# Optimization experiments

Hardware: AMD Instinct MI355X
Metric: run time of the kernel (lower is better)

The kernel has to match this reference:

```python
import jax, jax.numpy as jnp
import numpy as np

EPS = 1e-5
MAX_NORM = 1.0 - 1e-4

def _artanh(x):
    x = jnp.clip(x, -1.0 + 1e-5, 1.0 - 1e-5)
    return 0.5 * (jnp.log1p(x) - jnp.log1p(-x))

def _norm(x):
    return jnp.sqrt(jnp.maximum(jnp.sum(x * x, axis=-1, keepdims=True), EPS * EPS))

def _project(x):
    # clip points into the Poincare ball (c=1)
    n = _norm(x)
    return x * jnp.minimum(1.0, MAX_NORM / n)

def _logmap0(x):
    n = _norm(x)
    return _artanh(n) * x / n

def _expmap0(v):
    n = _norm(v)
    return jnp.tanh(n) * v / n

def _mobius_add(x, y):
    x2 = jnp.sum(x * x, -1, keepdims=True)
    y2 = jnp.sum(y * y, -1, keepdims=True)
    xy = jnp.sum(x * y, -1, keepdims=True)
    num = (1.0 + 2.0 * xy + y2) * x + (1.0 - x2) * y
    den = 1.0 + 2.0 * xy + x2 * y2
    return num / jnp.maximum(den, EPS)

def _mobius_matvec_all(W, x):
    # x: [B,T,D] on ball, W: [K,D,D] -> [B,T,K,D] (mx = x @ W[k].T for each expert k)
    mx = jnp.einsum('btd,ked->btke', x, W)
    xn = _norm(x)[:, :, None, :]            # [B,T,1,1]
    mn = _norm(mx)                          # [B,T,K,1]
    return jnp.tanh(mn / xn * _artanh(xn)) * mx / mn

def _depthwise_conv1d(x, w, b):
    # x: [B,T,C], w: [C,1,3] depthwise, padding=1
    y = jax.lax.conv_general_dilated(
        jnp.transpose(x, (0, 2, 1)), w, (1,), 'SAME',
        feature_group_count=x.shape[-1],
        dimension_numbers=('NCW', 'OIW', 'NCW'))
    return jnp.transpose(y, (0, 2, 1)) + b

def setup_inputs() -> dict:
    key = jax.random.key(0)
    ks = jax.random.split(key, 10)
    B, T, V, D, K, E, R = 8, 512, 50257, 64, 17, 32, 40
    return {
        'tokens': jax.random.randint(ks[0], (B, T), 0, V),
        'token_embed': 0.02 * jax.random.normal(ks[1], (V, D), jnp.float32),
        'conv_w': 0.3 * jax.random.normal(ks[2], (D, 1, 3), jnp.float32),
        'conv_b': jnp.zeros((D,), jnp.float32),
        'lin_w': 0.1 * jax.random.normal(ks[3], (D, K), jnp.float32),
        'lin_b': jnp.zeros((K,), jnp.float32),
        'exp_W': (1.0 / 8.0) * jax.random.normal(ks[4], (K, D, D), jnp.float32),
        'exp_bias': 0.01 * jax.random.normal(ks[5], (K, D), jnp.float32),
        'ln_gamma': jnp.ones((K, E), jnp.float32),
        'ln_beta': jnp.zeros((K, E), jnp.float32),
        'rel_T': jax.random.normal(ks[6], (R, E, E), jnp.float32),
        'rel_S': jax.random.normal(ks[7], (R, E, E), jnp.float32),
    }

def reference(tokens, token_embed, conv_w, conv_b, lin_w, lin_b,
              exp_W, exp_bias, ln_gamma, ln_beta, rel_T, rel_S):
    B, T = tokens.shape
    h0 = token_embed[tokens]                                  # [B,T,64]
    # TinyPosRouter: depthwise conv -> linear -> log_softmax
    hc = _depthwise_conv1d(h0, conv_w, conv_b)
    logp = jax.nn.log_softmax(hc @ lin_w + lin_b, axis=-1)    # [B,T,17]
    p = jnp.exp(logp)
    # round-trip through tangent space (as in source)
    x = _expmap0(_logmap0(_project(h0)))                      # [B,T,64]
    # all 17 hyperbolic experts, batched
    mv = _mobius_matvec_all(exp_W, x)                         # [B,T,17,64]
    y = _project(_mobius_add(mv, _project(exp_bias)))         # mobius bias add
    yt = _logmap0(y)                                          # tangent [B,T,17,64]
    a, g = jnp.split(yt, 2, axis=-1)
    y_glu = a * jax.nn.sigmoid(g)                             # [B,T,17,32]
    mu = jnp.mean(y_glu, -1, keepdims=True)
    var = jnp.var(y_glu, -1, keepdims=True)
    y_ln = (y_glu - mu) / jnp.sqrt(var + 1e-5) * ln_gamma + ln_beta
    y_out = _expmap0(y_ln)                                    # [B,T,17,32]
    y_avg = jnp.einsum('btke,btk->bte', y_out, p)             # soft routing
    # per-relation biaffine scores
    Th = jnp.einsum('btd,rde->brte', y_avg, rel_T)            # [B,40,T,32]
    Sd = jnp.einsum('btd,rde->brte', y_avg, rel_S)
    scores = jnp.einsum('brid,brjd->brij', Th, Sd) / Th.shape[-1]  # [B,40,T,T]
    score_rel = jnp.max(scores, axis=1)                       # [B,T,T]
    score_rel = jnp.where(jnp.eye(T, dtype=bool)[None], -1e9, score_rel)
    # greedy arborescence approximation: each dependent picks max-scoring head
    tree = jnp.argmax(score_rel, axis=1)                      # [B,T]
    return tree, score_rel, logp
```

## Files before the change

### kernel.cpp

```cpp
#include <hip/hip_runtime.h>
#include <hip/hip_bf16.h>
#include <math.h>

#define EPS   1e-5f
#define EPS2  (1e-5f * 1e-5f)
#define MAXN  (1.0f - 1e-4f)

typedef __attribute__((ext_vector_type(8))) short bf16x8;
typedef __attribute__((ext_vector_type(4))) float f32x4;

__device__ __forceinline__ float artanh_(float x) {
    x = fminf(fmaxf(x, -1.0f + 1e-5f), 1.0f - 1e-5f);
    return 0.5f * (log1pf(x) - log1pf(-x));
}
__device__ __forceinline__ float redw(float v) {
    #pragma unroll
    for (int m = 32; m >= 1; m >>= 1) v += __shfl_xor(v, m);
    return v;
}
__device__ __forceinline__ float red16(float v) {
    v += __shfl_xor(v, 1); v += __shfl_xor(v, 2);
    v += __shfl_xor(v, 4); v += __shfl_xor(v, 8);
    return v;
}
__device__ __forceinline__ float red8(float v) {
    v += __shfl_xor(v, 1); v += __shfl_xor(v, 2); v += __shfl_xor(v, 4);
    return v;
}
__device__ __forceinline__ float sigmoid_(float z) { return 1.0f / (1.0f + expf(-z)); }
__device__ __forceinline__ ushort f2bf(float f) {
    union { __hip_bfloat16 b; ushort u; } cv;
    cv.b = __float2bfloat16(f);
    return cv.u;
}
__device__ __forceinline__ bf16x8 pack8(float4 lo, float4 hi) {
    bf16x8 r;
    r[0] = (short)f2bf(lo.x); r[1] = (short)f2bf(lo.y);
    r[2] = (short)f2bf(lo.z); r[3] = (short)f2bf(lo.w);
    r[4] = (short)f2bf(hi.x); r[5] = (short)f2bf(hi.y);
    r[6] = (short)f2bf(hi.z); r[7] = (short)f2bf(hi.w);
    return r;
}

__global__ __launch_bounds__(256) void k1_token(
    const int* __restrict__ tokens, const float* __restrict__ emb,
    const float* __restrict__ conv_w, const float* __restrict__ conv_b,
    const float* __restrict__ lin_w, const float* __restrict__ lin_b,
    float* __restrict__ x_out, float* __restrict__ xn_out,
    float* __restrict__ p_out, float* __restrict__ logp_out)
{
    const int tok = blockIdx.x * 4 + (threadIdx.x >> 6);
    const int t   = tok & 511;
    const int c   = threadIdx.x & 63;

    const int id0 = tokens[tok];
    float h0 = emb[id0 * 64 + c];
    float hm = 0.0f, hp = 0.0f;
    if (t > 0)   hm = emb[tokens[tok - 1] * 64 + c];
    if (t < 511) hp = emb[tokens[tok + 1] * 64 + c];

    float hc = conv_w[c * 3 + 0] * hm + conv_w[c * 3 + 1] * h0 +
               conv_w[c * 3 + 2] * hp + conv_b[c];

    float myLg = 0.0f;
    #pragma unroll
    for (int j = 0; j < 17; ++j) {
        float v = redw(hc * lin_w[c * 17 + j]);
        if (c == j) myLg = v + lin_b[j];
    }
    float mx = (c < 17) ? myLg : -1e30f;
    #pragma unroll
    for (int m = 32; m >= 1; m >>= 1) mx = fmaxf(mx, __shfl_xor(mx, m));
    float ev = (c < 17) ? expf(myLg - mx) : 0.0f;
    float se = redw(ev);
    float lse = logf(se);
    if (c < 17) {
        float lp = myLg - mx - lse;
        logp_out[tok * 17 + c] = lp;
        p_out[tok * 17 + c]    = expf(lp);
    }

    float n0 = sqrtf(fmaxf(redw(h0 * h0), EPS2));
    float xp = h0 * fminf(1.0f, MAXN / n0);
    float n1 = sqrtf(fmaxf(redw(xp * xp), EPS2));
    float v1 = artanh_(n1) / n1 * xp;
    float n2 = sqrtf(fmaxf(redw(v1 * v1), EPS2));
    float xv = tanhf(n2) / n2 * v1;

    x_out[tok * 64 + c] = xv;
    float n3 = sqrtf(fmaxf(redw(xv * xv), EPS2));
    if (c == 0) xn_out[tok] = n3;
}

__global__ __launch_bounds__(256) void k2_expert(
    const float* __restrict__ x_in, const float* __restrict__ xn_in,
    const float* __restrict__ p_in, const float* __restrict__ expW,
    const float* __restrict__ expB, const float* __restrict__ g_in,
    const float* __restrict__ b_in, __hip_bfloat16* __restrict__ yk_out)
{
    __shared__ float mv_s[16][65];
    __shared__ float pb[64];
    __shared__ float gsk[32], bsk[32];
    __shared__ float p_sk[16];
    __shared__ float xn_s[16], axn_s[16];
    __shared__ float y2s_s;

    const int tid = threadIdx.x;
    const int l = tid & 63, w = tid >> 6;
    const int tg = tid >> 4, eg = tid & 15;
    const int k = blockIdx.x >> 8;
    const int chunk = blockIdx.x & 255;
    const int tok0 = chunk * 16;

    {
        const int d0 = (l >> 4) * 8;
        const float* ap = x_in + (tok0 + (l & 15)) * 64 + d0;
        const float* bp = expW + k * 4096 + (16 * w + (l & 15)) * 64 + d0;
        bf16x8 a0 = pack8(*reinterpret_cast<const float4*>(ap),
                          *reinterpret_cast<const float4*>(ap + 4));
        bf16x8 a1 = pack8(*reinterpret_cast<const float4*>(ap + 32),
                          *reinterpret_cast<const float4*>(ap + 36));
        bf16x8 b0 = pack8(*reinterpret_cast<const float4*>(bp),
                          *reinterpret_cast<const float4*>(bp + 4));
        bf16x8 b1 = pack8(*reinterpret_cast<const float4*>(bp + 32),
                          *reinterpret_cast<const float4*>(bp + 36));
        f32x4 acc = {0.f, 0.f, 0.f, 0.f};
        acc = __builtin_amdgcn_mfma_f32_16x16x32_bf16(a0, b0, acc, 0, 0, 0);
        acc = __builtin_amdgcn_mfma_f32_16x16x32_bf16(a1, b1, acc, 0, 0, 0);
        #pragma unroll
        for (int q = 0; q < 4; ++q)
            mv_s[(l >> 4) * 4 + q][16 * w + (l & 15)] = acc[q];
    }

    if (tid < 64) {
        float wv = expB[k * 64 + tid];
        float s = redw(wv * wv);
        float n = sqrtf(fmaxf(s, EPS2));
        float sc = fminf(1.0f, MAXN / n);
        pb[tid] = wv * sc;
        if (tid == 0) y2s_s = s * sc * sc;
    }
    if (tid >= 64 && tid < 96)  gsk[tid - 64] = g_in[k * 32 + (tid - 64)];
    if (tid >= 96 && tid < 128) bsk[tid - 96] = b_in[k * 32 + (tid - 96)];
    if (tid >= 128 && tid < 144) p_sk[tid - 128] = p_in[(tok0 + tid - 128) * 17 + k];
    if (tid >= 144 && tid < 160) {
        float xn = xn_in[tok0 + tid - 144];
        xn_s[tid - 144] = xn;
        axn_s[tid - 144] = artanh_(xn);
    }
    __syncthreads();

    const float xnv = xn_s[tg], axnv = axn_s[tg];
    float4 mvq = *reinterpret_cast<const float4*>(&mv_s[tg][eg * 4]);
    float mv0 = mvq.x, mv1 = mvq.y, mv2 = mvq.z, mv3 = mvq.w;

    float mn = sqrtf(fmaxf(red16(mv0*mv0 + mv1*mv1 + mv2*mv2 + mv3*mv3), EPS2));
    float tv = tanhf(mn / xnv * axnv);
    float cf = tv / mn;
    float xa0 = cf * mv0, xa1 = cf * mv1, xa2 = cf * mv2, xa3 = cf * mv3;
    float x2 = tv * tv;

    float4 pbv = *reinterpret_cast<const float4*>(&pb[eg * 4]);
    float xy = red16(xa0*pbv.x + xa1*pbv.y + xa2*pbv.z + xa3*pbv.w);
    float y2 = y2s_s;
    float ca = 1.0f + 2.0f * xy + y2;
    float cb = 1.0f - x2;
    float den = fmaxf(1.0f + 2.0f * xy + x2 * y2, EPS);
    float rden = 1.0f / den;
    float y0 = (ca * xa0 + cb * pbv.x) * rden;
    float y1 = (ca * xa1 + cb * pbv.y) * rden;
    float y2c = (ca * xa2 + cb * pbv.z) * rden;
    float y3 = (ca * xa3 + cb * pbv.w) * rden;

    float s2 = red16(y0*y0 + y1*y1 + y2c*y2c + y3*y3);
    float nP = sqrtf(fmaxf(s2, EPS2));
    float scP = fminf(1.0f, MAXN / nP);
    y0 *= scP; y1 *= scP; y2c *= scP; y3 *= scP;

    float n2 = sqrtf(fmaxf(s2 * scP * scP, EPS2));
    float lc = artanh_(n2) / n2;
    float yt0 = lc * y0, yt1 = lc * y1, yt2 = lc * y2c, yt3 = lc * y3;

    float pr0 = __shfl_xor(yt0, 8), pr1 = __shfl_xor(yt1, 8);
    float pr2 = __shfl_xor(yt2, 8), pr3 = __shfl_xor(yt3, 8);
    float gl0, gl1, gl2, gl3;
    if (eg < 8) {
        gl0 = yt0 * sigmoid_(pr0); gl1 = yt1 * sigmoid_(pr1);
        gl2 = yt2 * sigmoid_(pr2); gl3 = yt3 * sigmoid_(pr3);
    } else {
        gl0 = pr0 * sigmoid_(yt0); gl1 = pr1 * sigmoid_(yt1);
        gl2 = pr2 * sigmoid_(yt2); gl3 = pr3 * sigmoid_(yt3);
    }

    float mu = red8(gl0 + gl1 + gl2 + gl3) * (1.0f / 32.0f);
    float sq = red8(gl0*gl0 + gl1*gl1 + gl2*gl2 + gl3*gl3) * (1.0f / 32.0f);
    float rstd = rsqrtf(fmaxf(sq - mu * mu, 0.0f) + 1e-5f);
    int c0 = 4 * (eg & 7);
    float ln0 = (gl0 - mu) * rstd * gsk[c0 + 0] + bsk[c0 + 0];
    float ln1 = (gl1 - mu) * rstd * gsk[c0 + 1] + bsk[c0 + 1];
    float ln2 = (gl2 - mu) * rstd * gsk[c0 + 2] + bsk[c0 + 2];
    float ln3 = (gl3 - mu) * rstd * gsk[c0 + 3] + bsk[c0 + 3];

    float n3 = sqrtf(fmaxf(red8(ln0*ln0 + ln1*ln1 + ln2*ln2 + ln3*ln3), EPS2));
    float tc = tanhf(n3) / n3;

    float pk = p_sk[tg];
    float wq = pk * tc;

    if (eg < 8) {
        int tok = tok0 + tg;
        ushort4 o;
        o.x = f2bf(wq * ln0);
        o.y = f2bf(wq * ln1);
        o.z = f2bf(wq * ln2);
        o.w = f2bf(wq * ln3);
        *reinterpret_cast<ushort4*>(
            reinterpret_cast<ushort*>(yk_out) + ((size_t)tok * 17 + k) * 32 + c0) = o;
    }
}

__global__ __launch_bounds__(256) void k3_reduce(
    const __hip_bfloat16* __restrict__ yk, ushort* __restrict__ yab)
{
    int idx = blockIdx.x * 256 + threadIdx.x;
    int tok = idx >> 5, e = idx & 31;
    const __hip_bfloat16* p = yk + (size_t)tok * 17 * 32 + e;
    float s = 0.0f;
    #pragma unroll
    for (int k = 0; k < 17; ++k) s += __bfloat162float(p[k * 32]);
    yab[idx] = f2bf(s);
}

__global__ __launch_bounds__(256) void k4_rel(
    const ushort* __restrict__ yab, const float* __restrict__ relT,
    const float* __restrict__ relS, ushort* __restrict__ Z,
    unsigned long long* __restrict__ pmax)
{
    const int blk = blockIdx.x;
    const int b = blk / 160;
    const int rem = blk % 160;
    const int r = rem >> 2, tq = rem & 3;
    __shared__ float Ts[32][33], Ss[32][33], Mm[32][33];
    __shared__ float Zb[128][33];
    const int tid = threadIdx.x;
    const int l = tid & 63, w = tid >> 6;

    if (r == 0 && tid < 128)
        pmax[(size_t)b * 512 + tq * 128 + tid] = 0ull;

    {
        int d = tid >> 3, e0 = (tid & 7) * 4;
        float4 wT = *reinterpret_cast<const float4*>(&relT[r * 1024 + tid * 4]);
        float4 wS = *reinterpret_cast<const float4*>(&relS[r * 1024 + tid * 4]);
        Ts[d][e0 + 0] = wT.x; Ts[d][e0 + 1] = wT.y;
        Ts[d][e0 + 2] = wT.z; Ts[d][e0 + 3] = wT.w;
        Ss[d][e0 + 0] = wS.x; Ss[d][e0 + 1] = wS.y;
        Ss[d][e0 + 2] = wS.z; Ss[d][e0 + 3] = wS.w;
    }
    __syncthreads();

    {
        int d = tid >> 3, dp0 = (tid & 7) * 4;
        float m0 = 0.f, m1 = 0.f, m2 = 0.f, m3 = 0.f;
        #pragma unroll
        for (int e = 0; e < 32; ++e) {
            float tvv = Ts[d][e];
            m0 = fmaf(tvv, Ss[dp0 + 0][e], m0);
            m1 = fmaf(tvv, Ss[dp0 + 1][e], m1);
            m2 = fmaf(tvv, Ss[dp0 + 2][e], m2);
            m3 = fmaf(tvv, Ss[dp0 + 3][e], m3);
        }
        Mm[d][dp0 + 0] = m0; Mm[d][dp0 + 1] = m1;
        Mm[d][dp0 + 2] = m2; Mm[d][dp0 + 3] = m3;
    }
    __syncthreads();

    bf16x8 bm0, bm1;
    #pragma unroll
    for (int i = 0; i < 8; ++i) {
        int d = (l >> 4) * 8 + i;
        bm0[i] = (short)f2bf(Mm[d][(l & 15)]);
        bm1[i] = (short)f2bf(Mm[d][16 + (l & 15)]);
    }

    #pragma unroll
    for (int s = 0; s < 2; ++s) {
        int trow = tq * 128 + (w * 2 + s) * 16 + (l & 15);
        bf16x8 a = *reinterpret_cast<const bf16x8*>(
            yab + ((size_t)(b * 512) + trow) * 32 + (l >> 4) * 8);
        f32x4 acc0 = {0.f, 0.f, 0.f, 0.f}, acc1 = {0.f, 0.f, 0.f, 0.f};
        acc0 = __builtin_amdgcn_mfma_f32_16x16x32_bf16(a, bm0, acc0, 0, 0, 0);
        acc1 = __builtin_amdgcn_mfma_f32_16x16x32_bf16(a, bm1, acc1, 0, 0, 0);
        #pragma unroll
        for (int q = 0; q < 4; ++q) {
            int lr = (w * 2 + s) * 16 + (l >> 4) * 4 + q;
            Zb[lr][(l & 15)]      = acc0[q];
            Zb[lr][16 + (l & 15)] = acc1[q];
        }
    }
    __syncthreads();

    {
        int t2 = tid >> 1, half = tid & 1;
        union { ushort u[16]; uint4 q[2]; } pk;
        #pragma unroll
        for (int j = 0; j < 16; ++j) pk.u[j] = f2bf(Zb[t2][half * 16 + j]);
        size_t off = ((size_t)(b * 40 + r) * 512 + tq * 128 + t2) * 32 + half * 16;
        *reinterpret_cast<uint4*>(Z + off)     = pk.q[0];
        *reinterpret_cast<uint4*>(Z + off + 8) = pk.q[1];
    }
}

__global__ __launch_bounds__(1024) void k5_scores(
    const ushort* __restrict__ Z, const ushort* __restrict__ yab,
    float* __restrict__ score_out, unsigned long long* __restrict__ pmax)
{
    __shared__ float L[4][64][64];
    __shared__ unsigned long long pk_s[16][64];

    const int blk = blockIdx.x;
    const int b = blk >> 6, tile = blk & 63;
    const int it = (tile >> 3) * 64, jt = (tile & 7) * 64;
    const int w = threadIdx.x >> 6, lane = threadIdx.x & 63;
    const int q = w >> 2, s = w & 3;
    const int i0 = it + s * 16;
    const int arow = i0 + (lane & 15);
    const int koff = (lane >> 4) * 8;

    bf16x8 bb[4];
    #pragma unroll
    for (int c = 0; c < 4; ++c) {
        int jrow = jt + c * 16 + (lane & 15);
        bb[c] = *reinterpret_cast<const bf16x8*>(
            yab + ((size_t)(b * 512) + jrow) * 32 + koff);
    }

    f32x4 runmax[4];
    #pragma unroll
    for (int c = 0; c < 4; ++c)
        #pragma unroll
        for (int qq = 0; qq < 4; ++qq) runmax[c][qq] = -3.0e38f;

    const int r0 = q * 10;
    #pragma unroll 2
    for (int r = r0; r < r0 + 10; ++r) {
        bf16x8 a = *reinterpret_cast<const bf16x8*>(
            Z + ((size_t)(b * 40 + r) * 512 + arow) * 32 + koff);
        #pragma unroll
        for (int c = 0; c < 4; ++c) {
            f32x4 acc = {0.f, 0.f, 0.f, 0.f};
            acc = __builtin_amdgcn_mfma_f32_16x16x32_bf16(a, bb[c], acc, 0, 0, 0);
            #pragma unroll
            for (int qq = 0; qq < 4; ++qq) runmax[c][qq] = fmaxf(runmax[c][qq], acc[qq]);
        }
    }

    #pragma unroll
    for (int c = 0; c < 4; ++c) {
        #pragma unroll
        for (int qq = 0; qq < 4; ++qq) {
            int li = s * 16 + (lane >> 4) * 4 + qq;
            int lj = c * 16 + (lane & 15);
            L[q][li][lj] = runmax[c][qq];
        }
    }
    __syncthreads();

    {
        const int jl = threadIdx.x & 63, ig = threadIdx.x >> 6;
        const int gj = jt + jl;
        float bestv = -3.0e38f; int besti = it;
        #pragma unroll
        for (int p = 0; p < 4; ++p) {
            int i = ig + p * 16;
            float v = fmaxf(fmaxf(L[0][i][jl], L[1][i][jl]),
                            fmaxf(L[2][i][jl], L[3][i][jl])) * (1.0f / 32.0f);
            int gi = it + i;
            if (gi == gj) v = -1e9f;
            score_out[((size_t)b * 512 + gi) * 512 + gj] = v;
            if (v > bestv) { bestv = v; besti = gi; }
        }
        unsigned int ub = __float_as_uint(bestv);
        unsigned int ok = (ub >> 31) ? ~ub : (ub | 0x80000000u);
        pk_s[ig][jl] = ((unsigned long long)ok << 32) | (unsigned int)(511 - besti);
    }
    __syncthreads();
    if (threadIdx.x < 64) {
        unsigned long long best = pk_s[0][threadIdx.x];
        #pragma unroll
        for (int g = 1; g < 16; ++g) {
            unsigned long long v = pk_s[g][threadIdx.x];
            if (v > best) best = v;
        }
        atomicMax(&pmax[(size_t)b * 512 + jt + threadIdx.x], best);
    }
}

__global__ __launch_bounds__(256) void k6_tree(
    const unsigned long long* __restrict__ pmax, float* __restrict__ tree)
{
    int idx = blockIdx.x * 256 + threadIdx.x;
    tree[idx] = (float)(511 - (int)(pmax[idx] & 0x1ffull));
}

extern "C" void kernel_launch(void* const* d_in, const int* in_sizes, int n_in,
                              void* d_out, int out_size, void* d_ws, size_t ws_size,
                              hipStream_t stream)
{
    const int*   tokens  = (const int*)  d_in[0];
    const float* emb     = (const float*)d_in[1];
    const float* conv_w  = (const float*)d_in[2];
    const float* conv_b  = (const float*)d_in[3];
    const float* lin_w   = (const float*)d_in[4];
    const float* lin_b   = (const float*)d_in[5];
    const float* expW    = (const float*)d_in[6];
    const float* expB    = (const float*)d_in[7];
    const float* ln_g    = (const float*)d_in[8];
    const float* ln_b    = (const float*)d_in[9];
    const float* relT    = (const float*)d_in[10];
    const float* relS    = (const float*)d_in[11];

    float* out = (float*)d_out;
    float* tree_out  = out;
    float* score_out = out + 4096;
    float* logp_out  = out + 4096 + 2097152;

    float* ws = (float*)d_ws;
    float* x_ws  = ws;
    float* xn_ws = ws + 262144;
    float* p_ws  = ws + 266240;
    ushort* yab_ws = (ushort*)(ws + 335872);
    __hip_bfloat16* yk_ws = (__hip_bfloat16*)(ws + 401408);
    ushort* Z_ws = (ushort*)(ws + 1515520);
    unsigned long long* pmax_ws =
        (unsigned long long*)(ws + 4136960);

    k1_token<<<1024, 256, 0, stream>>>(tokens, emb, conv_w, conv_b, lin_w, lin_b,
                                       x_ws, xn_ws, p_ws, logp_out);
    k2_expert<<<4352, 256, 0, stream>>>(x_ws, xn_ws, p_ws, expW, expB, ln_g, ln_b, yk_ws);
    k3_reduce<<<512, 256, 0, stream>>>(yk_ws, yab_ws);
    k4_rel<<<1280, 256, 0, stream>>>(yab_ws, relT, relS, Z_ws, pmax_ws);
    k5_scores<<<512, 1024, 0, stream>>>(Z_ws, yab_ws, score_out, pmax_ws);
    k6_tree<<<16, 256, 0, stream>>>(pmax_ws, tree_out);
}
```

Before: 72.40 us.

## Restructure score kernel: full-relation loop per block, shuffle reduce, fuse tree argmax

The scores kernel now gives each block a 16-row strip covering all 512 columns and loops over all 40 relations per wave. This removes the cross-wave LDS max-combine and its syncs. yab for the batch is staged in padded LDS, the column argmax is reduced with wave shuffles before the atomicMax, and a last-block counter writes the tree output, so the separate k6 launch is gone. The trade-offs are fewer blocks (256 of 512 threads), longer serial MFMA chains per wave, and a threadfence/atomic completion protocol.

```diff
diff --git a/kernel.cpp b/kernel.cpp
--- a/kernel.cpp
+++ b/kernel.cpp
@@ -234,7 +234,7 @@
 __global__ __launch_bounds__(256) void k4_rel(
     const ushort* __restrict__ yab, const float* __restrict__ relT,
     const float* __restrict__ relS, ushort* __restrict__ Z,
-    unsigned long long* __restrict__ pmax)
+    unsigned long long* __restrict__ pmax, unsigned int* __restrict__ cnt)
 {
     const int blk = blockIdx.x;
     const int b = blk / 160;
@@ -247,6 +247,8 @@
 
     if (r == 0 && tid < 128)
         pmax[(size_t)b * 512 + tq * 128 + tid] = 0ull;
+    if (rem == 0 && tid == 128)
+        cnt[b] = 0u;
 
     {
         int d = tid >> 3, e0 = (tid & 7) * 4;
@@ -311,28 +313,37 @@
     }
 }
 
-__global__ __launch_bounds__(1024) void k5_scores(
+__global__ __launch_bounds__(512) void k5_scores(
     const ushort* __restrict__ Z, const ushort* __restrict__ yab,
-    float* __restrict__ score_out, unsigned long long* __restrict__ pmax)
-{
-    __shared__ float L[4][64][64];
-    __shared__ unsigned long long pk_s[16][64];
+    float* __restrict__ score_out, unsigned long long* __restrict__ pmax,
+    unsigned int* __restrict__ cnt, float* __restrict__ tree)
+{
+    __shared__ ushort yls[512 * 40];
+    __shared__ unsigned int last_s;
 
     const int blk = blockIdx.x;
-    const int b = blk >> 6, tile = blk & 63;
-    const int it = (tile >> 3) * 64, jt = (tile & 7) * 64;
-    const int w = threadIdx.x >> 6, lane = threadIdx.x & 63;
-    const int q = w >> 2, s = w & 3;
-    const int i0 = it + s * 16;
-    const int arow = i0 + (lane & 15);
+    const int b = blk >> 5, it = (blk & 31) * 16;
+    const int tid = threadIdx.x;
+    const int w = tid >> 6, lane = tid & 63;
+    const int jseg = w * 64;
     const int koff = (lane >> 4) * 8;
 
+    {
+        const uint4* src = reinterpret_cast<const uint4*>(
+            yab + ((size_t)b * 512 + tid) * 32);
+        ushort* row = &yls[tid * 40];
+        *reinterpret_cast<uint4*>(row)      = src[0];
+        *reinterpret_cast<uint4*>(row + 8)  = src[1];
+        *reinterpret_cast<uint4*>(row + 16) = src[2];
+        *reinterpret_cast<uint4*>(row + 24) = src[3];
+    }
+    __syncthreads();
+
     bf16x8 bb[4];
     #pragma unroll
     for (int c = 0; c < 4; ++c) {
-        int jrow = jt + c * 16 + (lane & 15);
-        bb[c] = *reinterpret_cast<const bf16x8*>(
-            yab + ((size_t)(b * 512) + jrow) * 32 + koff);
+        int jrow = jseg + c * 16 + (lane & 15);
+        bb[c] = *reinterpret_cast<const bf16x8*>(&yls[jrow * 40 + koff]);
     }
 
     f32x4 runmax[4];
@@ -341,11 +352,11 @@
         #pragma unroll
         for (int qq = 0; qq < 4; ++qq) runmax[c][qq] = -3.0e38f;
 
-    const int r0 = q * 10;
-    #pragma unroll 2
-    for (int r = r0; r < r0 + 10; ++r) {
-        bf16x8 a = *reinterpret_cast<const bf16x8*>(
-            Z + ((size_t)(b * 40 + r) * 512 + arow) * 32 + koff);
+    const ushort* Zbase =
+        Z + ((size_t)(b * 40) * 512 + it + (lane & 15)) * 32 + koff;
+    #pragma unroll 4
+    for (int r = 0; r < 40; ++r) {
+        bf16x8 a = *reinterpret_cast<const bf16x8*>(Zbase + (size_t)r * 512 * 32);
         #pragma unroll
         for (int c = 0; c < 4; ++c) {
             f32x4 acc = {0.f, 0.f, 0.f, 0.f};
@@ -357,50 +368,33 @@
 
     #pragma unroll
     for (int c = 0; c < 4; ++c) {
-        #pragma unroll
-        for (int qq = 0; qq < 4; ++qq) {
-            int li = s * 16 + (lane >> 4) * 4 + qq;
-            int lj = c * 16 + (lane & 15);
-            L[q][li][lj] = runmax[c][qq];
-        }
-    }
-    __syncthreads();
-
-    {
-        const int jl = threadIdx.x & 63, ig = threadIdx.x >> 6;
-        const int gj = jt + jl;
-        float bestv = -3.0e38f; int besti = it;
-        #pragma unroll
-        for (int p = 0; p < 4; ++p) {
-            int i = ig + p * 16;
-            float v = fmaxf(fmaxf(L[0][i][jl], L[1][i][jl]),
-                            fmaxf(L[2][i][jl], L[3][i][jl])) * (1.0f / 32.0f);
-            int gi = it + i;
+        const int gj = jseg + c * 16 + (lane & 15);
+        float bestv = -3.0e38f; int besti = 0;
+        #pragma unroll
+        for (int q = 0; q < 4; ++q) {
+            int gi = it + (lane >> 4) * 4 + q;
+            float v = runmax[c][q] * (1.0f / 32.0f);
             if (gi == gj) v = -1e9f;
             score_out[((size_t)b * 512 + gi) * 512 + gj] = v;
             if (v > bestv) { bestv = v; besti = gi; }
         }
         unsigned int ub = __float_as_uint(bestv);
         unsigned int ok = (ub >> 31) ? ~ub : (ub | 0x80000000u);
-        pk_s[ig][jl] = ((unsigned long long)ok << 32) | (unsigned int)(511 - besti);
-    }
-    __syncthreads();
-    if (threadIdx.x < 64) {
-        unsigned long long best = pk_s[0][threadIdx.x];
-        #pragma unroll
-        for (int g = 1; g < 16; ++g) {
-            unsigned long long v = pk_s[g][threadIdx.x];
-            if (v > best) best = v;
-        }
-        atomicMax(&pmax[(size_t)b * 512 + jt + threadIdx.x], best);
-    }
-}
-
-__global__ __launch_bounds__(256) void k6_tree(
-    const unsigned long long* __restrict__ pmax, float* __restrict__ tree)
-{
-    int idx = blockIdx.x * 256 + threadIdx.x;
-    tree[idx] = (float)(511 - (int)(pmax[idx] & 0x1ffull));
+        unsigned long long key =
+            ((unsigned long long)ok << 32) | (unsigned int)(511 - besti);
+        unsigned long long o1 = __shfl_xor(key, 16); if (o1 > key) key = o1;
+        unsigned long long o2 = __shfl_xor(key, 32); if (o2 > key) key = o2;
+        if ((lane >> 4) == 0)
+            atomicMax(&pmax[(size_t)b * 512 + gj], key);
+    }
+
+    __syncthreads();
+    if (tid == 0) { __threadfence(); last_s = atomicAdd(&cnt[b], 1u); }
+    __syncthreads();
+    if (last_s == 31u) {
+        unsigned long long key = atomicMax(&pmax[(size_t)b * 512 + tid], 0ull);
+        tree[b * 512 + tid] = (float)(511 - (int)(key & 0x1ffull));
+    }
 }
 
 extern "C" void kernel_launch(void* const* d_in, const int* in_sizes, int n_in,
@@ -434,12 +428,12 @@
     ushort* Z_ws = (ushort*)(ws + 1515520);
     unsigned long long* pmax_ws =
         (unsigned long long*)(ws + 4136960);
+    unsigned int* cnt_ws = (unsigned int*)(ws + 4145152);
 
     k1_token<<<1024, 256, 0, stream>>>(tokens, emb, conv_w, conv_b, lin_w, lin_b,
                                        x_ws, xn_ws, p_ws, logp_out);
     k2_expert<<<4352, 256, 0, stream>>>(x_ws, xn_ws, p_ws, expW, expB, ln_g, ln_b, yk_ws);
     k3_reduce<<<512, 256, 0, stream>>>(yk_ws, yab_ws);
-    k4_rel<<<1280, 256, 0, stream>>>(yab_ws, relT, relS, Z_ws, pmax_ws);
-    k5_scores<<<512, 1024, 0, stream>>>(Z_ws, yab_ws, score_out, pmax_ws);
-    k6_tree<<<16, 256, 0, stream>>>(pmax_ws, tree_out);
-}
+    k4_rel<<<1280, 256, 0, stream>>>(yab_ws, relT, relS, Z_ws, pmax_ws, cnt_ws);
+    k5_scores<<<256, 512, 0, stream>>>(Z_ws, yab_ws, score_out, pmax_ws, cnt_ws, tree_out);
+}
```

Result: slower. 76.03 us (+5.0%).
